# Performance work log

Measured on AMD Instinct MI355X. Metric: run time of the kernel, lower is better.

## Reference

```python
import jax, jax.numpy as jnp
import numpy as np

H = 2048   # hidden_size
I = 4096   # intermediate_size (expert_dim_per_shard, world_size=1)
E = 8      # num_local_experts


def setup_inputs() -> dict:
    key = jax.random.key(0)
    ks = jax.random.split(key, 7)
    s = 0.02
    return {
        "hidden_states": jax.random.normal(ks[0], (1, 2048, H), dtype=jnp.float32),
        "router_w": jax.random.normal(ks[1], (H, E), dtype=jnp.float32) * s,
        "gate_up_proj": jax.random.normal(ks[2], (E, H, 2 * I), dtype=jnp.float32) * s,
        "down_proj": jax.random.normal(ks[3], (E, I, H), dtype=jnp.float32) * s,
        "shared_gate_w": jax.random.normal(ks[4], (H, I), dtype=jnp.float32) * s,
        "shared_up_w": jax.random.normal(ks[5], (H, I), dtype=jnp.float32) * s,
        "shared_down_w": jax.random.normal(ks[6], (I, H), dtype=jnp.float32) * s,
        "top_k": 1,
    }


def reference(hidden_states, router_w, gate_up_proj, down_proj,
              shared_gate_w, shared_up_w, shared_down_w, top_k):
    b, s, h = hidden_states.shape
    hs = hidden_states.reshape(-1, h)                      # [T, H]
    T = hs.shape[0]

    # router + topk scatter (non-topk -> -inf so sigmoid -> 0)
    logits = hs @ router_w                                 # [T, E]
    top_v, top_i = jax.lax.top_k(logits, top_k)            # [T, k]
    neg_inf = jnp.full_like(logits, -jnp.inf)
    rows = jnp.arange(T)[:, None]
    router_scores = neg_inf.at[rows, top_i].set(top_v).T   # [E, T]
    router_scores = jax.nn.sigmoid(router_scores.astype(jnp.float32)).astype(hs.dtype)

    # dense dispatch: every token to every expert, scaled by (mostly zero) scores
    routed_in = hs[None, :, :] * router_scores[:, :, None]  # [E, T, H]

    # per-expert grouped GEMM (SwiGLU)
    gate_up = jnp.einsum('eth,ehf->etf', routed_in, gate_up_proj)  # [E, T, 2I]
    gate, up = jnp.split(gate_up, 2, axis=-1)
    routed_out = jnp.einsum('eti,eih->eth', up * jax.nn.silu(gate), down_proj)  # [E, T, H]

    # shared expert (SwiGLU MLP)
    shared = (jax.nn.silu(hs @ shared_gate_w) * (hs @ shared_up_w)) @ shared_down_w  # [T, H]

    # scatter_add over arange indices == sum over experts
    out = shared + routed_out.sum(axis=0)                  # [T, H]
    return out, router_scores
```

## Files before the change

### kernel.cpp

```cpp
#include <hip/hip_runtime.h>
#include <hip/hip_bf16.h>

#define H_DIM 2048
#define E_NUM 8
#define I_DIM 4096
#define TWO_I 8192
#define T_TOK 2048

#define BM 256
#define BN 64
#define BK 64

typedef __bf16 bf16x8 __attribute__((ext_vector_type(8)));
typedef float f32x4 __attribute__((ext_vector_type(4)));

static __device__ __forceinline__ unsigned short f2bs(float x) {
    __hip_bfloat16 h = __float2bfloat16(x);
    return __builtin_bit_cast(unsigned short, h);
}

#define GLL(gsrc, ldst) __builtin_amdgcn_global_load_lds( \
    (const __attribute__((address_space(1))) void*)(gsrc), \
    (__attribute__((address_space(3))) void*)(ldst), 16, 0, 0)

#define MFMA16(a, b, c) __builtin_amdgcn_mfma_f32_16x16x32_bf16(a, b, c, 0, 0, 0)
#define BSWZ(n) (((((n) & 7) ^ (((n) >> 2) & 7))) << 4)
#define A_SRC_CHUNK(lane) ((((lane) & 7) ^ (((lane) >> 3) & 7)) * 8)
#define BARRIER() asm volatile("s_waitcnt lgkmcnt(0)\ns_barrier" ::: "memory")

static __device__ __forceinline__ bf16x8 bload(
    const unsigned short* __restrict__ Bs, int n, int s, int h) {
    int off = (n * 128 + s * 64 + h * 16) ^ BSWZ(n);
    return *reinterpret_cast<const bf16x8*>((const char*)Bs + off);
}

static __device__ __forceinline__ bf16x8 aload(
    const unsigned short* __restrict__ As, int row, int s, int h) {
    int off = row * 128 + ((s * 64 + h * 16) ^ ((row & 7) << 4));
    return *reinterpret_cast<const bf16x8*>((const char*)As + off);
}

__global__ __launch_bounds__(256) void router_convert_kernel(
    const float* __restrict__ hs, const float* __restrict__ rw,
    float* __restrict__ out_scores, int* __restrict__ eidx,
    unsigned short* __restrict__ xb, unsigned short* __restrict__ xs) {
    int tok = blockIdx.x * 4 + (threadIdx.x >> 6);
    int lane = threadIdx.x & 63;
    const float* row = hs + (size_t)tok * H_DIM;
    float4 v[8];
    float acc[E_NUM];
#pragma unroll
    for (int e = 0; e < E_NUM; e++) acc[e] = 0.f;
#pragma unroll
    for (int i = 0; i < 8; i++) {
        int hb = i * 256 + lane * 4;
        v[i] = *reinterpret_cast<const float4*>(row + hb);
        const float* w0 = rw + (size_t)hb * E_NUM;
#pragma unroll
        for (int e = 0; e < E_NUM; e++) {
            acc[e] += v[i].x * w0[e] + v[i].y * w0[E_NUM + e] +
                      v[i].z * w0[2 * E_NUM + e] + v[i].w * w0[3 * E_NUM + e];
        }
    }
#pragma unroll
    for (int e = 0; e < E_NUM; e++) {
#pragma unroll
        for (int o = 32; o > 0; o >>= 1) acc[e] += __shfl_xor(acc[e], o, 64);
    }
    int best = 0; float bv = acc[0];
#pragma unroll
    for (int e = 1; e < E_NUM; e++) { if (acc[e] > bv) { bv = acc[e]; best = e; } }
    float sc = 1.f / (1.f + expf(-bv));
    if (lane < E_NUM) out_scores[(size_t)lane * T_TOK + tok] = (lane == best) ? sc : 0.f;
    if (lane == 0) eidx[tok] = best;
    unsigned short* xbr = xb + (size_t)tok * H_DIM;
    unsigned short* xsr = xs + (size_t)tok * H_DIM;
#pragma unroll
    for (int i = 0; i < 8; i++) {
        int hb = i * 256 + lane * 4;
        ushort4 b, s4;
        b.x = f2bs(v[i].x); b.y = f2bs(v[i].y); b.z = f2bs(v[i].z); b.w = f2bs(v[i].w);
        s4.x = f2bs(v[i].x * sc); s4.y = f2bs(v[i].y * sc);
        s4.z = f2bs(v[i].z * sc); s4.w = f2bs(v[i].w * sc);
        *reinterpret_cast<ushort4*>(xbr + hb) = b;
        *reinterpret_cast<ushort4*>(xsr + hb) = s4;
    }
}

__global__ void group_kernel(const int* __restrict__ eidx, int* __restrict__ perm,
                             int* __restrict__ off) {
    __shared__ int cnt[E_NUM];
    __shared__ int base[E_NUM];
    int t = threadIdx.x;
    if (t < E_NUM) cnt[t] = 0;
    __syncthreads();
    for (int i = t; i < T_TOK; i += 256) atomicAdd(&cnt[eidx[i]], 1);
    __syncthreads();
    if (t == 0) {
        int s = 0;
        for (int e = 0; e < E_NUM; e++) { base[e] = s; off[e] = s; s += cnt[e]; }
        off[E_NUM] = s;
    }
    __syncthreads();
    for (int i = t; i < T_TOK; i += 256) {
        int e = eidx[i];
        int p = atomicAdd(&base[e], 1);
        perm[p] = i;
    }
}

__global__ __launch_bounds__(512, 4) void gemm1_kernel(
    const unsigned short* __restrict__ xb, const unsigned short* __restrict__ xs,
    const float* __restrict__ gup, const float* __restrict__ sg,
    const float* __restrict__ su, const int* __restrict__ perm,
    const int* __restrict__ off, unsigned short* __restrict__ hmid) {
    int nt = blockIdx.x;
    int g = blockIdx.y >> 3;
    int mt = blockIdx.y & 7;
    int rowbase, ng;
    if (g < E_NUM) { rowbase = off[g]; ng = off[g + 1] - rowbase; }
    else { rowbase = 0; ng = T_TOK; }
    int mstart = mt * BM;
    if (mstart >= ng) return;

    __shared__ unsigned short As[2][BM * BK];
    __shared__ unsigned short Bg[BN * BK];
    __shared__ unsigned short Bu[BN * BK];

    int tid = threadIdx.x;
    int wave = tid >> 6, lane = tid & 63;
    int h = lane >> 4, ln = lane & 15;

    const unsigned short* Abase = (g == E_NUM) ? xb : xs;
    unsigned int aoff[4];
#pragma unroll
    for (int j = 0; j < 4; j++) {
        int r = wave * 32 + j * 8 + (lane >> 3);
        int sr = mstart + r; sr = (sr < ng) ? sr : (ng - 1);
        int tokr = (g < E_NUM) ? perm[rowbase + sr] : sr;
        aoff[j] = (unsigned int)tokr * H_DIM + A_SRC_CHUNK(lane);
    }
    int n0 = nt * BN;
    const float* gbase;
    const float* ubase;
    size_t ldb;
    if (g < E_NUM) {
        gbase = gup + (size_t)g * H_DIM * TWO_I + n0;
        ubase = gbase + I_DIM;
        ldb = TWO_I;
    } else {
        gbase = sg + n0;
        ubase = su + n0;
        ldb = I_DIM;
    }
    int k0i = (tid >> 4) * 2;
    int nb = (tid & 15) * 4;
    const float* pg = gbase + (size_t)k0i * ldb + nb;
    const float* pu = ubase + (size_t)k0i * ldb + nb;

    f32x4 zero = {0.f, 0.f, 0.f, 0.f};
    f32x4 accg[2][4], accu[2][4];
#pragma unroll
    for (int i = 0; i < 2; i++)
#pragma unroll
        for (int j = 0; j < 4; j++) { accg[i][j] = zero; accu[i][j] = zero; }

    const int NT = H_DIM / BK;
    f32x4 qg0, qg1, qu0, qu1;

#define G1_QLOAD(t_) { size_t ko_ = (size_t)(t_) * BK * ldb; \
        qg0 = *reinterpret_cast<const f32x4*>(pg + ko_); \
        qg1 = *reinterpret_cast<const f32x4*>(pg + ko_ + ldb); \
        qu0 = *reinterpret_cast<const f32x4*>(pu + ko_); \
        qu1 = *reinterpret_cast<const f32x4*>(pu + ko_ + ldb); }
#define G1_BWRITE() { _Pragma("unroll") \
        for (int i_ = 0; i_ < 4; i_++) { int n_ = nb + i_; \
            unsigned og_ = (unsigned)f2bs(qg0[i_]) | ((unsigned)f2bs(qg1[i_]) << 16); \
            unsigned ou_ = (unsigned)f2bs(qu0[i_]) | ((unsigned)f2bs(qu1[i_]) << 16); \
            int ob_ = (n_ * 128 + k0i * 2) ^ BSWZ(n_); \
            *reinterpret_cast<unsigned*>((char*)Bg + ob_) = og_; \
            *reinterpret_cast<unsigned*>((char*)Bu + ob_) = ou_; } }
#define G1_AGLL(t_, buf_) { _Pragma("unroll") \
        for (int j_ = 0; j_ < 4; j_++) \
            GLL(Abase + aoff[j_] + (unsigned)(t_) * BK, \
                &As[buf_][(wave * 32 + j_ * 8) * BK]); }

    G1_QLOAD(0);
    G1_AGLL(0, 0);
    asm volatile("s_waitcnt vmcnt(0)" ::: "memory");
    G1_BWRITE();
    G1_AGLL(1, 1);
    G1_QLOAD(1);
    BARRIER();

    for (int t = 0; t < NT; ++t) {
        const unsigned short* Ab = &As[t & 1][0];
#pragma unroll
        for (int s = 0; s < 2; s++) {
            bf16x8 a0 = aload(Ab, wave * 32 + 0 * 16 + ln, s, h);
            bf16x8 a1 = aload(Ab, wave * 32 + 1 * 16 + ln, s, h);
#pragma unroll
            for (int j = 0; j < 4; j++) {
                bf16x8 bg = bload(Bg, j * 16 + ln, s, h);
                accg[0][j] = MFMA16(a0, bg, accg[0][j]);
                accg[1][j] = MFMA16(a1, bg, accg[1][j]);
            }
#pragma unroll
            for (int j = 0; j < 4; j++) {
                bf16x8 bu = bload(Bu, j * 16 + ln, s, h);
                accu[0][j] = MFMA16(a0, bu, accu[0][j]);
                accu[1][j] = MFMA16(a1, bu, accu[1][j]);
            }
        }
        BARRIER();
        if (t + 1 < NT) {
            G1_BWRITE();
            int tc = t + 2; if (tc > NT - 1) tc = NT - 1;
            G1_AGLL(tc, t & 1);
            G1_QLOAD(tc);
            BARRIER();
        }
    }

    int hbase = (g < E_NUM) ? rowbase : T_TOK;
#pragma unroll
    for (int i = 0; i < 2; i++) {
#pragma unroll
        for (int j = 0; j < 4; j++) {
#pragma unroll
            for (int r = 0; r < 4; r++) {
                int row = wave * 32 + i * 16 + h * 4 + r;
                int sr = mstart + row;
                if (sr < ng) {
                    float gv = accg[i][j][r], uv = accu[i][j][r];
                    float hv = gv / (1.f + expf(-gv)) * uv;
                    int col = n0 + j * 16 + ln;
                    hmid[(size_t)(hbase + sr) * I_DIM + col] = f2bs(hv);
                }
            }
        }
    }
}

template <int ADD>
__global__ __launch_bounds__(512, 4) void gemm2_kernel(
    const unsigned short* __restrict__ hmid, const float* __restrict__ dwn,
    const float* __restrict__ sd, const int* __restrict__ perm,
    const int* __restrict__ off, float* __restrict__ out) {
    int nt = blockIdx.x;
    int g, mt, rowbase, ng, hbase;
    if (ADD) {
        g = blockIdx.y >> 3; mt = blockIdx.y & 7;
        rowbase = off[g]; ng = off[g + 1] - rowbase; hbase = rowbase;
    } else {
        g = E_NUM; mt = blockIdx.y; rowbase = 0; ng = T_TOK; hbase = T_TOK;
    }
    int mstart = mt * BM;
    if (mstart >= ng) return;

    __shared__ unsigned short As[2][BM * BK];
    __shared__ unsigned short Bs[BN * BK];

    int tid = threadIdx.x;
    int wave = tid >> 6, lane = tid & 63;
    int h = lane >> 4, ln = lane & 15;

    unsigned int aoff[4];
#pragma unroll
    for (int j = 0; j < 4; j++) {
        int r = wave * 32 + j * 8 + (lane >> 3);
        int sr = mstart + r; sr = (sr < ng) ? sr : (ng - 1);
        aoff[j] = (unsigned int)(hbase + sr) * I_DIM + A_SRC_CHUNK(lane);
    }
    int n0 = nt * BN;
    const float* bbase = ADD ? (dwn + (size_t)g * I_DIM * H_DIM + n0) : (sd + n0);
    const size_t ldb = H_DIM;
    int k0i = (tid >> 4) * 2;
    int nb = (tid & 15) * 4;
    const float* pb = bbase + (size_t)k0i * ldb + nb;

    f32x4 zero = {0.f, 0.f, 0.f, 0.f};
    f32x4 acc[2][4];
#pragma unroll
    for (int i = 0; i < 2; i++)
#pragma unroll
        for (int j = 0; j < 4; j++) acc[i][j] = zero;

    const int NT2 = I_DIM / BK;
    f32x4 qb0, qb1;

#define G2_QLOAD(t_) { size_t ko_ = (size_t)(t_) * BK * ldb; \
        qb0 = *reinterpret_cast<const f32x4*>(pb + ko_); \
        qb1 = *reinterpret_cast<const f32x4*>(pb + ko_ + ldb); }
#define G2_BWRITE() { _Pragma("unroll") \
        for (int i_ = 0; i_ < 4; i_++) { int n_ = nb + i_; \
            unsigned o_ = (unsigned)f2bs(qb0[i_]) | ((unsigned)f2bs(qb1[i_]) << 16); \
            int ob_ = (n_ * 128 + k0i * 2) ^ BSWZ(n_); \
            *reinterpret_cast<unsigned*>((char*)Bs + ob_) = o_; } }
#define G2_AGLL(t_, buf_) { _Pragma("unroll") \
        for (int j_ = 0; j_ < 4; j_++) \
            GLL(hmid + aoff[j_] + (unsigned)(t_) * BK, \
                &As[buf_][(wave * 32 + j_ * 8) * BK]); }

    G2_QLOAD(0);
    G2_AGLL(0, 0);
    asm volatile("s_waitcnt vmcnt(0)" ::: "memory");
    G2_BWRITE();
    G2_AGLL(1, 1);
    G2_QLOAD(1);
    BARRIER();

    for (int t = 0; t < NT2; ++t) {
        const unsigned short* Ab = &As[t & 1][0];
#pragma unroll
        for (int s = 0; s < 2; s++) {
            bf16x8 a0 = aload(Ab, wave * 32 + 0 * 16 + ln, s, h);
            bf16x8 a1 = aload(Ab, wave * 32 + 1 * 16 + ln, s, h);
#pragma unroll
            for (int j = 0; j < 4; j++) {
                bf16x8 b = bload(Bs, j * 16 + ln, s, h);
                acc[0][j] = MFMA16(a0, b, acc[0][j]);
                acc[1][j] = MFMA16(a1, b, acc[1][j]);
            }
        }
        BARRIER();
        if (t + 1 < NT2) {
            G2_BWRITE();
            int tc = t + 2; if (tc > NT2 - 1) tc = NT2 - 1;
            G2_AGLL(tc, t & 1);
            G2_QLOAD(tc);
            BARRIER();
        }
    }

#pragma unroll
    for (int i = 0; i < 2; i++) {
#pragma unroll
        for (int j = 0; j < 4; j++) {
#pragma unroll
            for (int r = 0; r < 4; r++) {
                int row = wave * 32 + i * 16 + h * 4 + r;
                int sr = mstart + row;
                if (sr < ng) {
                    int tok = ADD ? perm[rowbase + sr] : sr;
                    int col = n0 + j * 16 + ln;
                    float v = acc[i][j][r];
                    float* o = out + (size_t)tok * H_DIM + col;
                    if (ADD) *o += v; else *o = v;
                }
            }
        }
    }
}

extern "C" void kernel_launch(void* const* d_in, const int* in_sizes, int n_in,
                              void* d_out, int out_size, void* d_ws, size_t ws_size,
                              hipStream_t stream) {
    (void)in_sizes; (void)n_in; (void)out_size;
    const float* hs  = (const float*)d_in[0];
    const float* rw  = (const float*)d_in[1];
    const float* gup = (const float*)d_in[2];
    const float* dwn = (const float*)d_in[3];
    const float* sg  = (const float*)d_in[4];
    const float* su  = (const float*)d_in[5];
    const float* sd  = (const float*)d_in[6];
    float* out = (float*)d_out;
    float* out_scores = out + (size_t)T_TOK * H_DIM;

    char* w = (char*)d_ws;
    size_t o = 0;
    auto alloc = [&](size_t bytes) {
        void* p = w + o;
        o += (bytes + 255) & ~(size_t)255;
        return p;
    };
    unsigned short* xb   = (unsigned short*)alloc((size_t)T_TOK * H_DIM * 2);
    unsigned short* xs   = (unsigned short*)alloc((size_t)T_TOK * H_DIM * 2);
    unsigned short* hmid = (unsigned short*)alloc((size_t)2 * T_TOK * I_DIM * 2);
    int* eidx    = (int*)alloc(T_TOK * 4);
    int* perm    = (int*)alloc(T_TOK * 4);
    int* off     = (int*)alloc(64 * 4);
    if (ws_size < o) return;

    router_convert_kernel<<<T_TOK / 4, 256, 0, stream>>>(hs, rw, out_scores, eidx, xb, xs);
    group_kernel<<<1, 256, 0, stream>>>(eidx, perm, off);

    gemm1_kernel<<<dim3(I_DIM / BN, 9 * 8), 512, 0, stream>>>(
        xb, xs, gup, sg, su, perm, off, hmid);
    gemm2_kernel<0><<<dim3(H_DIM / BN, 8), 512, 0, stream>>>(hmid, dwn, sd, perm, off, out);
    gemm2_kernel<1><<<dim3(H_DIM / BN, E_NUM * 8), 512, 0, stream>>>(hmid, dwn, sd, perm, off, out);
}
```

Measured before the change: 488.7 us.

## Halve M tile to 128 and apply router score in GEMM1 epilogue

Shrinks the M tile from 256 to 128 rows, so each wave computes a single 16-row MFMA strip, the grids gain twice as many M tiles, and the occupancy hint rises to 6. The scaled copy of the activations (xs) is dropped. The router score is stored per token and applied to the gate and up accumulators in the GEMM1 epilogue, which removes a bf16 write and read of the activations. Smaller tiles mean each fp32 weight tile is converted and reused across fewer rows, so the weight-side traffic per FLOP roughly doubles. The gain comes from better load balance across the small, uneven expert groups.

```diff
diff --git a/kernel.cpp b/kernel.cpp
--- a/kernel.cpp
+++ b/kernel.cpp
@@ -7,7 +7,7 @@
 #define TWO_I 8192
 #define T_TOK 2048
 
-#define BM 256
+#define BM 128
 #define BN 64
 #define BK 64
 
@@ -43,7 +43,7 @@
 __global__ __launch_bounds__(256) void router_convert_kernel(
     const float* __restrict__ hs, const float* __restrict__ rw,
     float* __restrict__ out_scores, int* __restrict__ eidx,
-    unsigned short* __restrict__ xb, unsigned short* __restrict__ xs) {
+    float* __restrict__ score, unsigned short* __restrict__ xb) {
     int tok = blockIdx.x * 4 + (threadIdx.x >> 6);
     int lane = threadIdx.x & 63;
     const float* row = hs + (size_t)tok * H_DIM;
@@ -72,18 +72,14 @@
     for (int e = 1; e < E_NUM; e++) { if (acc[e] > bv) { bv = acc[e]; best = e; } }
     float sc = 1.f / (1.f + expf(-bv));
     if (lane < E_NUM) out_scores[(size_t)lane * T_TOK + tok] = (lane == best) ? sc : 0.f;
-    if (lane == 0) eidx[tok] = best;
+    if (lane == 0) { eidx[tok] = best; score[tok] = sc; }
     unsigned short* xbr = xb + (size_t)tok * H_DIM;
-    unsigned short* xsr = xs + (size_t)tok * H_DIM;
 #pragma unroll
     for (int i = 0; i < 8; i++) {
         int hb = i * 256 + lane * 4;
-        ushort4 b, s4;
+        ushort4 b;
         b.x = f2bs(v[i].x); b.y = f2bs(v[i].y); b.z = f2bs(v[i].z); b.w = f2bs(v[i].w);
-        s4.x = f2bs(v[i].x * sc); s4.y = f2bs(v[i].y * sc);
-        s4.z = f2bs(v[i].z * sc); s4.w = f2bs(v[i].w * sc);
         *reinterpret_cast<ushort4*>(xbr + hb) = b;
-        *reinterpret_cast<ushort4*>(xsr + hb) = s4;
     }
 }
 
@@ -109,14 +105,14 @@
     }
 }
 
-__global__ __launch_bounds__(512, 4) void gemm1_kernel(
-    const unsigned short* __restrict__ xb, const unsigned short* __restrict__ xs,
-    const float* __restrict__ gup, const float* __restrict__ sg,
-    const float* __restrict__ su, const int* __restrict__ perm,
-    const int* __restrict__ off, unsigned short* __restrict__ hmid) {
+__global__ __launch_bounds__(512, 6) void gemm1_kernel(
+    const unsigned short* __restrict__ xb, const float* __restrict__ gup,
+    const float* __restrict__ sg, const float* __restrict__ su,
+    const int* __restrict__ perm, const int* __restrict__ off,
+    const float* __restrict__ score, unsigned short* __restrict__ hmid) {
     int nt = blockIdx.x;
-    int g = blockIdx.y >> 3;
-    int mt = blockIdx.y & 7;
+    int g = blockIdx.y >> 4;
+    int mt = blockIdx.y & 15;
     int rowbase, ng;
     if (g < E_NUM) { rowbase = off[g]; ng = off[g + 1] - rowbase; }
     else { rowbase = 0; ng = T_TOK; }
@@ -131,11 +127,10 @@
     int wave = tid >> 6, lane = tid & 63;
     int h = lane >> 4, ln = lane & 15;
 
-    const unsigned short* Abase = (g == E_NUM) ? xb : xs;
-    unsigned int aoff[4];
-#pragma unroll
-    for (int j = 0; j < 4; j++) {
-        int r = wave * 32 + j * 8 + (lane >> 3);
+    unsigned int aoff[2];
+#pragma unroll
+    for (int j = 0; j < 2; j++) {
+        int r = wave * 16 + j * 8 + (lane >> 3);
         int sr = mstart + r; sr = (sr < ng) ? sr : (ng - 1);
         int tokr = (g < E_NUM) ? perm[rowbase + sr] : sr;
         aoff[j] = (unsigned int)tokr * H_DIM + A_SRC_CHUNK(lane);
@@ -159,11 +154,9 @@
     const float* pu = ubase + (size_t)k0i * ldb + nb;
 
     f32x4 zero = {0.f, 0.f, 0.f, 0.f};
-    f32x4 accg[2][4], accu[2][4];
-#pragma unroll
-    for (int i = 0; i < 2; i++)
-#pragma unroll
-        for (int j = 0; j < 4; j++) { accg[i][j] = zero; accu[i][j] = zero; }
+    f32x4 accg[4], accu[4];
+#pragma unroll
+    for (int j = 0; j < 4; j++) { accg[j] = zero; accu[j] = zero; }
 
     const int NT = H_DIM / BK;
     f32x4 qg0, qg1, qu0, qu1;
@@ -181,9 +174,9 @@
             *reinterpret_cast<unsigned*>((char*)Bg + ob_) = og_; \
             *reinterpret_cast<unsigned*>((char*)Bu + ob_) = ou_; } }
 #define G1_AGLL(t_, buf_) { _Pragma("unroll") \
-        for (int j_ = 0; j_ < 4; j_++) \
-            GLL(Abase + aoff[j_] + (unsigned)(t_) * BK, \
-                &As[buf_][(wave * 32 + j_ * 8) * BK]); }
+        for (int j_ = 0; j_ < 2; j_++) \
+            GLL(xb + aoff[j_] + (unsigned)(t_) * BK, \
+                &As[buf_][(wave * 16 + j_ * 8) * BK]); }
 
     G1_QLOAD(0);
     G1_AGLL(0, 0);
@@ -197,19 +190,16 @@
         const unsigned short* Ab = &As[t & 1][0];
 #pragma unroll
         for (int s = 0; s < 2; s++) {
-            bf16x8 a0 = aload(Ab, wave * 32 + 0 * 16 + ln, s, h);
-            bf16x8 a1 = aload(Ab, wave * 32 + 1 * 16 + ln, s, h);
+            bf16x8 a0 = aload(Ab, wave * 16 + ln, s, h);
 #pragma unroll
             for (int j = 0; j < 4; j++) {
                 bf16x8 bg = bload(Bg, j * 16 + ln, s, h);
-                accg[0][j] = MFMA16(a0, bg, accg[0][j]);
-                accg[1][j] = MFMA16(a1, bg, accg[1][j]);
+                accg[j] = MFMA16(a0, bg, accg[j]);
             }
 #pragma unroll
             for (int j = 0; j < 4; j++) {
                 bf16x8 bu = bload(Bu, j * 16 + ln, s, h);
-                accu[0][j] = MFMA16(a0, bu, accu[0][j]);
-                accu[1][j] = MFMA16(a1, bu, accu[1][j]);
+                accu[j] = MFMA16(a0, bu, accu[j]);
             }
         }
         BARRIER();
@@ -224,33 +214,32 @@
 
     int hbase = (g < E_NUM) ? rowbase : T_TOK;
 #pragma unroll
-    for (int i = 0; i < 2; i++) {
-#pragma unroll
-        for (int j = 0; j < 4; j++) {
-#pragma unroll
-            for (int r = 0; r < 4; r++) {
-                int row = wave * 32 + i * 16 + h * 4 + r;
-                int sr = mstart + row;
-                if (sr < ng) {
-                    float gv = accg[i][j][r], uv = accu[i][j][r];
-                    float hv = gv / (1.f + expf(-gv)) * uv;
-                    int col = n0 + j * 16 + ln;
-                    hmid[(size_t)(hbase + sr) * I_DIM + col] = f2bs(hv);
-                }
+    for (int r = 0; r < 4; r++) {
+        int row = wave * 16 + h * 4 + r;
+        int sr = mstart + row;
+        if (sr < ng) {
+            float sc = 1.f;
+            if (g < E_NUM) sc = score[perm[rowbase + sr]];
+#pragma unroll
+            for (int j = 0; j < 4; j++) {
+                float gv = accg[j][r] * sc, uv = accu[j][r] * sc;
+                float hv = gv / (1.f + expf(-gv)) * uv;
+                int col = n0 + j * 16 + ln;
+                hmid[(size_t)(hbase + sr) * I_DIM + col] = f2bs(hv);
             }
         }
     }
 }
 
 template <int ADD>
-__global__ __launch_bounds__(512, 4) void gemm2_kernel(
+__global__ __launch_bounds__(512, 6) void gemm2_kernel(
     const unsigned short* __restrict__ hmid, const float* __restrict__ dwn,
     const float* __restrict__ sd, const int* __restrict__ perm,
     const int* __restrict__ off, float* __restrict__ out) {
     int nt = blockIdx.x;
     int g, mt, rowbase, ng, hbase;
     if (ADD) {
-        g = blockIdx.y >> 3; mt = blockIdx.y & 7;
+        g = blockIdx.y >> 4; mt = blockIdx.y & 15;
         rowbase = off[g]; ng = off[g + 1] - rowbase; hbase = rowbase;
     } else {
         g = E_NUM; mt = blockIdx.y; rowbase = 0; ng = T_TOK; hbase = T_TOK;
@@ -265,10 +254,10 @@
     int wave = tid >> 6, lane = tid & 63;
     int h = lane >> 4, ln = lane & 15;
 
-    unsigned int aoff[4];
-#pragma unroll
-    for (int j = 0; j < 4; j++) {
-        int r = wave * 32 + j * 8 + (lane >> 3);
+    unsigned int aoff[2];
+#pragma unroll
+    for (int j = 0; j < 2; j++) {
+        int r = wave * 16 + j * 8 + (lane >> 3);
         int sr = mstart + r; sr = (sr < ng) ? sr : (ng - 1);
         aoff[j] = (unsigned int)(hbase + sr) * I_DIM + A_SRC_CHUNK(lane);
     }
@@ -280,11 +269,9 @@
     const float* pb = bbase + (size_t)k0i * ldb + nb;
 
     f32x4 zero = {0.f, 0.f, 0.f, 0.f};
-    f32x4 acc[2][4];
-#pragma unroll
-    for (int i = 0; i < 2; i++)
-#pragma unroll
-        for (int j = 0; j < 4; j++) acc[i][j] = zero;
+    f32x4 acc[4];
+#pragma unroll
+    for (int j = 0; j < 4; j++) acc[j] = zero;
 
     const int NT2 = I_DIM / BK;
     f32x4 qb0, qb1;
@@ -298,9 +285,9 @@
             int ob_ = (n_ * 128 + k0i * 2) ^ BSWZ(n_); \
             *reinterpret_cast<unsigned*>((char*)Bs + ob_) = o_; } }
 #define G2_AGLL(t_, buf_) { _Pragma("unroll") \
-        for (int j_ = 0; j_ < 4; j_++) \
+        for (int j_ = 0; j_ < 2; j_++) \
             GLL(hmid + aoff[j_] + (unsigned)(t_) * BK, \
-                &As[buf_][(wave * 32 + j_ * 8) * BK]); }
+                &As[buf_][(wave * 16 + j_ * 8) * BK]); }
 
     G2_QLOAD(0);
     G2_AGLL(0, 0);
@@ -314,13 +301,11 @@
         const unsigned short* Ab = &As[t & 1][0];
 #pragma unroll
         for (int s = 0; s < 2; s++) {
-            bf16x8 a0 = aload(Ab, wave * 32 + 0 * 16 + ln, s, h);
-            bf16x8 a1 = aload(Ab, wave * 32 + 1 * 16 + ln, s, h);
+            bf16x8 a0 = aload(Ab, wave * 16 + ln, s, h);
 #pragma unroll
             for (int j = 0; j < 4; j++) {
                 bf16x8 b = bload(Bs, j * 16 + ln, s, h);
-                acc[0][j] = MFMA16(a0, b, acc[0][j]);
-                acc[1][j] = MFMA16(a1, b, acc[1][j]);
+                acc[j] = MFMA16(a0, b, acc[j]);
             }
         }
         BARRIER();
@@ -334,20 +319,17 @@
     }
 
 #pragma unroll
-    for (int i = 0; i < 2; i++) {
-#pragma unroll
-        for (int j = 0; j < 4; j++) {
-#pragma unroll
-            for (int r = 0; r < 4; r++) {
-                int row = wave * 32 + i * 16 + h * 4 + r;
-                int sr = mstart + row;
-                if (sr < ng) {
-                    int tok = ADD ? perm[rowbase + sr] : sr;
-                    int col = n0 + j * 16 + ln;
-                    float v = acc[i][j][r];
-                    float* o = out + (size_t)tok * H_DIM + col;
-                    if (ADD) *o += v; else *o = v;
-                }
+    for (int r = 0; r < 4; r++) {
+        int row = wave * 16 + h * 4 + r;
+        int sr = mstart + row;
+        if (sr < ng) {
+            int tok = ADD ? perm[rowbase + sr] : sr;
+#pragma unroll
+            for (int j = 0; j < 4; j++) {
+                int col = n0 + j * 16 + ln;
+                float v = acc[j][r];
+                float* o = out + (size_t)tok * H_DIM + col;
+                if (ADD) *o += v; else *o = v;
             }
         }
     }
@@ -375,18 +357,18 @@
         return p;
     };
     unsigned short* xb   = (unsigned short*)alloc((size_t)T_TOK * H_DIM * 2);
-    unsigned short* xs   = (unsigned short*)alloc((size_t)T_TOK * H_DIM * 2);
     unsigned short* hmid = (unsigned short*)alloc((size_t)2 * T_TOK * I_DIM * 2);
+    float* score = (float*)alloc(T_TOK * 4);
     int* eidx    = (int*)alloc(T_TOK * 4);
     int* perm    = (int*)alloc(T_TOK * 4);
     int* off     = (int*)alloc(64 * 4);
     if (ws_size < o) return;
 
-    router_convert_kernel<<<T_TOK / 4, 256, 0, stream>>>(hs, rw, out_scores, eidx, xb, xs);
+    router_convert_kernel<<<T_TOK / 4, 256, 0, stream>>>(hs, rw, out_scores, eidx, score, xb);
     group_kernel<<<1, 256, 0, stream>>>(eidx, perm, off);
 
-    gemm1_kernel<<<dim3(I_DIM / BN, 9 * 8), 512, 0, stream>>>(
-        xb, xs, gup, sg, su, perm, off, hmid);
-    gemm2_kernel<0><<<dim3(H_DIM / BN, 8), 512, 0, stream>>>(hmid, dwn, sd, perm, off, out);
-    gemm2_kernel<1><<<dim3(H_DIM / BN, E_NUM * 8), 512, 0, stream>>>(hmid, dwn, sd, perm, off, out);
-}
+    gemm1_kernel<<<dim3(I_DIM / BN, 9 * 16), 512, 0, stream>>>(
+        xb, gup, sg, su, perm, off, score, hmid);
+    gemm2_kernel<0><<<dim3(H_DIM / BN, 16), 512, 0, stream>>>(hmid, dwn, sd, perm, off, out);
+    gemm2_kernel<1><<<dim3(H_DIM / BN, E_NUM * 16), 512, 0, stream>>>(hmid, dwn, sd, perm, off, out);
+}
```

New measurement: 540.6 us. 1.11x slower.

## Fold router score into gemm1 epilogue and merge down-proj launches with atomics

Applied to the files above, without the earlier changes.

Drops the separately scaled bf16 copy of the activations and applies the sigmoid router score to the gate/up accumulators in the gemm1 epilogue, which saves one activation write and lets routed and shared GEMM1 read the same input. Merges the shared and routed down-projection launches into one grid that accumulates into a zeroed output with float atomics, so the two no longer serialize. In exchange it adds a memset and atomic read-modify-write traffic, and the float summation order becomes nondeterministic. Scaling after the GEMM rather than before also changes bf16 rounding slightly.

```diff
diff --git a/kernel.cpp b/kernel.cpp
--- a/kernel.cpp
+++ b/kernel.cpp
@@ -43,7 +43,7 @@
 __global__ __launch_bounds__(256) void router_convert_kernel(
     const float* __restrict__ hs, const float* __restrict__ rw,
     float* __restrict__ out_scores, int* __restrict__ eidx,
-    unsigned short* __restrict__ xb, unsigned short* __restrict__ xs) {
+    float* __restrict__ score, unsigned short* __restrict__ xb) {
     int tok = blockIdx.x * 4 + (threadIdx.x >> 6);
     int lane = threadIdx.x & 63;
     const float* row = hs + (size_t)tok * H_DIM;
@@ -72,18 +72,14 @@
     for (int e = 1; e < E_NUM; e++) { if (acc[e] > bv) { bv = acc[e]; best = e; } }
     float sc = 1.f / (1.f + expf(-bv));
     if (lane < E_NUM) out_scores[(size_t)lane * T_TOK + tok] = (lane == best) ? sc : 0.f;
-    if (lane == 0) eidx[tok] = best;
+    if (lane == 0) { eidx[tok] = best; score[tok] = sc; }
     unsigned short* xbr = xb + (size_t)tok * H_DIM;
-    unsigned short* xsr = xs + (size_t)tok * H_DIM;
 #pragma unroll
     for (int i = 0; i < 8; i++) {
         int hb = i * 256 + lane * 4;
-        ushort4 b, s4;
+        ushort4 b;
         b.x = f2bs(v[i].x); b.y = f2bs(v[i].y); b.z = f2bs(v[i].z); b.w = f2bs(v[i].w);
-        s4.x = f2bs(v[i].x * sc); s4.y = f2bs(v[i].y * sc);
-        s4.z = f2bs(v[i].z * sc); s4.w = f2bs(v[i].w * sc);
         *reinterpret_cast<ushort4*>(xbr + hb) = b;
-        *reinterpret_cast<ushort4*>(xsr + hb) = s4;
     }
 }
 
@@ -110,10 +106,10 @@
 }
 
 __global__ __launch_bounds__(512, 4) void gemm1_kernel(
-    const unsigned short* __restrict__ xb, const unsigned short* __restrict__ xs,
-    const float* __restrict__ gup, const float* __restrict__ sg,
-    const float* __restrict__ su, const int* __restrict__ perm,
-    const int* __restrict__ off, unsigned short* __restrict__ hmid) {
+    const unsigned short* __restrict__ xb, const float* __restrict__ gup,
+    const float* __restrict__ sg, const float* __restrict__ su,
+    const int* __restrict__ perm, const int* __restrict__ off,
+    const float* __restrict__ score, unsigned short* __restrict__ hmid) {
     int nt = blockIdx.x;
     int g = blockIdx.y >> 3;
     int mt = blockIdx.y & 7;
@@ -131,7 +127,6 @@
     int wave = tid >> 6, lane = tid & 63;
     int h = lane >> 4, ln = lane & 15;
 
-    const unsigned short* Abase = (g == E_NUM) ? xb : xs;
     unsigned int aoff[4];
 #pragma unroll
     for (int j = 0; j < 4; j++) {
@@ -182,7 +177,7 @@
             *reinterpret_cast<unsigned*>((char*)Bu + ob_) = ou_; } }
 #define G1_AGLL(t_, buf_) { _Pragma("unroll") \
         for (int j_ = 0; j_ < 4; j_++) \
-            GLL(Abase + aoff[j_] + (unsigned)(t_) * BK, \
+            GLL(xb + aoff[j_] + (unsigned)(t_) * BK, \
                 &As[buf_][(wave * 32 + j_ * 8) * BK]); }
 
     G1_QLOAD(0);
@@ -226,13 +221,14 @@
 #pragma unroll
     for (int i = 0; i < 2; i++) {
 #pragma unroll
-        for (int j = 0; j < 4; j++) {
-#pragma unroll
-            for (int r = 0; r < 4; r++) {
-                int row = wave * 32 + i * 16 + h * 4 + r;
-                int sr = mstart + row;
-                if (sr < ng) {
-                    float gv = accg[i][j][r], uv = accu[i][j][r];
+        for (int r = 0; r < 4; r++) {
+            int row = wave * 32 + i * 16 + h * 4 + r;
+            int sr = mstart + row;
+            if (sr < ng) {
+                float sc = (g < E_NUM) ? score[perm[rowbase + sr]] : 1.f;
+#pragma unroll
+                for (int j = 0; j < 4; j++) {
+                    float gv = accg[i][j][r] * sc, uv = accu[i][j][r] * sc;
                     float hv = gv / (1.f + expf(-gv)) * uv;
                     int col = n0 + j * 16 + ln;
                     hmid[(size_t)(hbase + sr) * I_DIM + col] = f2bs(hv);
@@ -242,19 +238,16 @@
     }
 }
 
-template <int ADD>
 __global__ __launch_bounds__(512, 4) void gemm2_kernel(
     const unsigned short* __restrict__ hmid, const float* __restrict__ dwn,
     const float* __restrict__ sd, const int* __restrict__ perm,
     const int* __restrict__ off, float* __restrict__ out) {
     int nt = blockIdx.x;
-    int g, mt, rowbase, ng, hbase;
-    if (ADD) {
-        g = blockIdx.y >> 3; mt = blockIdx.y & 7;
-        rowbase = off[g]; ng = off[g + 1] - rowbase; hbase = rowbase;
-    } else {
-        g = E_NUM; mt = blockIdx.y; rowbase = 0; ng = T_TOK; hbase = T_TOK;
-    }
+    int g = blockIdx.y >> 3;
+    int mt = blockIdx.y & 7;
+    int rowbase, ng, hbase;
+    if (g < E_NUM) { rowbase = off[g]; ng = off[g + 1] - rowbase; hbase = rowbase; }
+    else { rowbase = 0; ng = T_TOK; hbase = T_TOK; }
     int mstart = mt * BM;
     if (mstart >= ng) return;
 
@@ -273,7 +266,7 @@
         aoff[j] = (unsigned int)(hbase + sr) * I_DIM + A_SRC_CHUNK(lane);
     }
     int n0 = nt * BN;
-    const float* bbase = ADD ? (dwn + (size_t)g * I_DIM * H_DIM + n0) : (sd + n0);
+    const float* bbase = (g < E_NUM) ? (dwn + (size_t)g * I_DIM * H_DIM + n0) : (sd + n0);
     const size_t ldb = H_DIM;
     int k0i = (tid >> 4) * 2;
     int nb = (tid & 15) * 4;
@@ -336,17 +329,15 @@
 #pragma unroll
     for (int i = 0; i < 2; i++) {
 #pragma unroll
-        for (int j = 0; j < 4; j++) {
-#pragma unroll
-            for (int r = 0; r < 4; r++) {
-                int row = wave * 32 + i * 16 + h * 4 + r;
-                int sr = mstart + row;
-                if (sr < ng) {
-                    int tok = ADD ? perm[rowbase + sr] : sr;
+        for (int r = 0; r < 4; r++) {
+            int row = wave * 32 + i * 16 + h * 4 + r;
+            int sr = mstart + row;
+            if (sr < ng) {
+                int tok = (g < E_NUM) ? perm[rowbase + sr] : sr;
+#pragma unroll
+                for (int j = 0; j < 4; j++) {
                     int col = n0 + j * 16 + ln;
-                    float v = acc[i][j][r];
-                    float* o = out + (size_t)tok * H_DIM + col;
-                    if (ADD) *o += v; else *o = v;
+                    atomicAdd(out + (size_t)tok * H_DIM + col, acc[i][j][r]);
                 }
             }
         }
@@ -375,18 +366,20 @@
         return p;
     };
     unsigned short* xb   = (unsigned short*)alloc((size_t)T_TOK * H_DIM * 2);
-    unsigned short* xs   = (unsigned short*)alloc((size_t)T_TOK * H_DIM * 2);
     unsigned short* hmid = (unsigned short*)alloc((size_t)2 * T_TOK * I_DIM * 2);
+    float* score = (float*)alloc(T_TOK * 4);
     int* eidx    = (int*)alloc(T_TOK * 4);
     int* perm    = (int*)alloc(T_TOK * 4);
     int* off     = (int*)alloc(64 * 4);
     if (ws_size < o) return;
 
-    router_convert_kernel<<<T_TOK / 4, 256, 0, stream>>>(hs, rw, out_scores, eidx, xb, xs);
+    hipMemsetAsync(out, 0, (size_t)T_TOK * H_DIM * sizeof(float), stream);
+
+    router_convert_kernel<<<T_TOK / 4, 256, 0, stream>>>(hs, rw, out_scores, eidx, score, xb);
     group_kernel<<<1, 256, 0, stream>>>(eidx, perm, off);
 
     gemm1_kernel<<<dim3(I_DIM / BN, 9 * 8), 512, 0, stream>>>(
-        xb, xs, gup, sg, su, perm, off, hmid);
-    gemm2_kernel<0><<<dim3(H_DIM / BN, 8), 512, 0, stream>>>(hmid, dwn, sd, perm, off, out);
-    gemm2_kernel<1><<<dim3(H_DIM / BN, E_NUM * 8), 512, 0, stream>>>(hmid, dwn, sd, perm, off, out);
-}
+        xb, gup, sg, su, perm, off, score, hmid);
+    gemm2_kernel<<<dim3(H_DIM / BN, 9 * 8), 512, 0, stream>>>(
+        hmid, dwn, sd, perm, off, out);
+}
```

Result: faster. 473.3 us (-3.2%).
